# Optimization experiments

Measured on AMD Instinct MI355X. Metric: run time of the kernel, lower is better.

Reference implementation:

```python
import jax, jax.numpy as jnp
import numpy as np

KERNEL = 3
PAD = 1
STRIDE = 1

def setup_inputs() -> dict:
    key = jax.random.key(0)
    k1, k2 = jax.random.split(key)
    x = jax.random.normal(k1, (32, 128, 56, 56), dtype=jnp.float32)
    # xavier_uniform-like init for weight
    fan_in = 128 * KERNEL * KERNEL
    fan_out = 256 * KERNEL * KERNEL
    limit = float(np.sqrt(6.0 / (fan_in + fan_out)))
    weight = jax.random.uniform(k2, (256, 128, KERNEL, KERNEL), dtype=jnp.float32,
                                minval=-limit, maxval=limit)
    bias = jnp.zeros((256,), dtype=jnp.float32)
    return {"x": x, "weight": weight, "bias": bias}

def reference(x, weight, bias):
    # Equivalent to the per-pixel im2col matmul loop: a standard 3x3 conv,
    # stride 1, symmetric padding 1, plus per-channel bias.
    out = jax.lax.conv_general_dilated(
        x, weight,
        window_strides=(STRIDE, STRIDE),
        padding=((PAD, PAD), (PAD, PAD)),
        dimension_numbers=("NCHW", "OIHW", "NCHW"),
    )
    return out + bias[None, :, None, None]
```

## Files before the change

### kernel.cpp

```cpp
#include <hip/hip_runtime.h>
#include <hip/hip_bf16.h>
#include <stdint.h>
#include <stddef.h>

#define NIMG 32
#define C_IN 128
#define C_OUT 256
#define HW 56
#define SP 3136
#define STOT (NIMG * SP)
#define PD 58
#define KTOT 1152

#define BM 256
#define BN 256
#define BK 64
#define NKT (KTOT / BK)
#define THREADS 512

typedef __attribute__((ext_vector_type(8))) short bf16x8;
typedef __attribute__((ext_vector_type(4))) float f32x4;

__device__ __forceinline__ void gload16(const void* g, void* l) {
    __builtin_amdgcn_global_load_lds(
        (const __attribute__((address_space(1))) void*)g,
        (__attribute__((address_space(3))) void*)l,
        16, 0, 0);
}

#define BAR() do { asm volatile("" ::: "memory"); \
                   __builtin_amdgcn_s_barrier();  \
                   asm volatile("" ::: "memory"); } while (0)
#define LGKM0() do { asm volatile("s_waitcnt lgkmcnt(0)" ::: "memory"); \
                     __builtin_amdgcn_sched_barrier(0); } while (0)
#define VMCNT(n) do { asm volatile("s_waitcnt vmcnt(" #n ")" ::: "memory"); \
                      __builtin_amdgcn_sched_barrier(0); } while (0)

__device__ __forceinline__ unsigned short bf2u(float f) {
    __hip_bfloat16 b = __float2bfloat16(f);
    return *reinterpret_cast<unsigned short*>(&b);
}

__global__ __launch_bounds__(256)
void pad_transpose_kernel(const float* __restrict__ x,
                          __hip_bfloat16* __restrict__ xp) {
    __shared__ float t[C_IN][HW + 1];
    const int hp = blockIdx.x % PD;
    const int n  = blockIdx.x / PD;
    const int h  = hp - 1;
    const bool interior = ((unsigned)h < (unsigned)HW);
    if (interior) {
        for (int idx = threadIdx.x; idx < C_IN * HW; idx += 256) {
            int ci = idx / HW, w = idx - ci * HW;
            t[ci][w] = x[((size_t)n * C_IN + ci) * SP + h * HW + w];
        }
    }
    __syncthreads();
    ushort4* dst = (ushort4*)(xp + ((size_t)n * PD + hp) * PD * C_IN);
    for (int idx = threadIdx.x; idx < PD * C_IN / 4; idx += 256) {
        int el = idx * 4;
        int wp = el >> 7, c0 = el & 127;
        ushort4 v = {0, 0, 0, 0};
        if (interior && wp >= 1 && wp <= HW) {
            int w = wp - 1;
            v.x = bf2u(t[c0 + 0][w]);
            v.y = bf2u(t[c0 + 1][w]);
            v.z = bf2u(t[c0 + 2][w]);
            v.w = bf2u(t[c0 + 3][w]);
        }
        dst[idx] = v;
    }
}

__global__ void wt_transform_kernel(const float* __restrict__ wgt,
                                    __hip_bfloat16* __restrict__ wt) {
    int idx = blockIdx.x * 256 + threadIdx.x;
    int ci  = idx & 127;
    int co  = (idx >> 7) & 255;
    int tap = idx >> 15;
    wt[idx] = __float2bfloat16(wgt[(co * C_IN + ci) * 9 + tap]);
}

__global__ __launch_bounds__(THREADS, 2)
void conv_mfma_kernel(const __hip_bfloat16* __restrict__ xp,
                      const __hip_bfloat16* __restrict__ wt,
                      const float* __restrict__ bias,
                      float* __restrict__ out) {
    extern __shared__ short smem[];

    const int tid  = threadIdx.x;
    const int lane = tid & 63;
    const int wid  = tid >> 6;
    const int s0   = blockIdx.x * BN;

    const int cg_el = (((lane & 3) ^ ((lane >> 3) & 3)) << 3);
    const int srow  = wid * 16 + (lane >> 2);
    const int aS0   = srow * C_IN + cg_el;
    const int aS1   = aS0 + 128 * C_IN;
    int s_r = s0 + srow;
    int n_  = s_r / SP, rem = s_r - n_ * SP;
    int h_  = rem / HW, w_ = rem - h_ * HW;
    const int bS0 = ((n_ * PD + h_) * PD + w_) * C_IN + cg_el;
    s_r += 128;
    n_ = s_r / SP; rem = s_r - n_ * SP; h_ = rem / HW; w_ = rem - h_ * HW;
    const int bS1 = ((n_ * PD + h_) * PD + w_) * C_IN + cg_el;
    const int ldsw = wid * 512;

    const int rl  = lane & 15;
    const int rch = (((lane >> 4) ^ ((lane >> 1) & 3)) << 3);
    const int wm  = (wid >> 2) * 128;
    const int wn  = (wid & 3) * 64;
    const int aRd = (wm + rl) * 32 + rch;
    const int bRd = (wn + rl) * 32 + rch;

    auto STG_A = [&](int kt, int kk, int bf) {
        int t2 = (kt >= NKT) ? kt - NKT : kt;
        int tap = t2 >> 1;
        const __hip_bfloat16* src =
            wt + tap * (C_OUT * C_IN) + ((t2 & 1) << 6) + (kk << 5);
        short* d = smem + bf * 32768 + kk * 8192 + ldsw;
        gload16(src + aS0, d);
        gload16(src + aS1, d + 4096);
    };
    auto STG_B = [&](int kt, int kk, int bf) {
        int t2 = (kt >= NKT) ? kt - NKT : kt;
        int tap = t2 >> 1;
        int kh = (tap * 11) >> 5, kw = tap - kh * 3;
        const __hip_bfloat16* src =
            xp + (kh * PD + kw) * C_IN + ((t2 & 1) << 6) + (kk << 5);
        short* d = smem + bf * 32768 + 16384 + kk * 8192 + ldsw;
        gload16(src + bS0, d);
        gload16(src + bS1, d + 4096);
    };

    f32x4 acc[8][4] = {};

    STG_A(0, 0, 0); STG_B(0, 0, 0);
    STG_A(0, 1, 0); STG_B(0, 1, 0);
    STG_A(1, 0, 1); STG_B(1, 0, 1);
    VMCNT(4);
    BAR();

    for (int t = 0; t < NKT; ++t) {
        const int b = t & 1;
        const short* Ak0 = smem + b * 32768;
        const short* Ak1 = Ak0 + 8192;
        const short* Bk0 = Ak0 + 16384;
        const short* Bk1 = Ak0 + 24576;
        bf16x8 af[4], bfr[4];

        #pragma unroll
        for (int j = 0; j < 4; ++j) af[j]  = *(const bf16x8*)(Ak0 + aRd + j * 512);
        #pragma unroll
        for (int j = 0; j < 4; ++j) bfr[j] = *(const bf16x8*)(Bk0 + bRd + j * 512);
        STG_A(t + 1, 1, b ^ 1);
        BAR(); LGKM0();
        __builtin_amdgcn_s_setprio(1);
        #pragma unroll
        for (int mi = 0; mi < 4; ++mi)
            #pragma unroll
            for (int ni = 0; ni < 4; ++ni)
                acc[mi][ni] = __builtin_amdgcn_mfma_f32_16x16x32_bf16(
                    af[mi], bfr[ni], acc[mi][ni], 0, 0, 0);
        __builtin_amdgcn_s_setprio(0);
        BAR();

        #pragma unroll
        for (int j = 0; j < 4; ++j) af[j] = *(const bf16x8*)(Ak0 + aRd + 2048 + j * 512);
        STG_B(t + 1, 1, b ^ 1);
        BAR(); LGKM0();
        __builtin_amdgcn_s_setprio(1);
        #pragma unroll
        for (int mi = 0; mi < 4; ++mi)
            #pragma unroll
            for (int ni = 0; ni < 4; ++ni)
                acc[4 + mi][ni] = __builtin_amdgcn_mfma_f32_16x16x32_bf16(
                    af[mi], bfr[ni], acc[4 + mi][ni], 0, 0, 0);
        __builtin_amdgcn_s_setprio(0);
        BAR();

        #pragma unroll
        for (int j = 0; j < 4; ++j) af[j]  = *(const bf16x8*)(Ak1 + aRd + j * 512);
        #pragma unroll
        for (int j = 0; j < 4; ++j) bfr[j] = *(const bf16x8*)(Bk1 + bRd + j * 512);
        STG_A(t + 2, 0, b);
        BAR(); LGKM0();
        __builtin_amdgcn_s_setprio(1);
        #pragma unroll
        for (int mi = 0; mi < 4; ++mi)
            #pragma unroll
            for (int ni = 0; ni < 4; ++ni)
                acc[mi][ni] = __builtin_amdgcn_mfma_f32_16x16x32_bf16(
                    af[mi], bfr[ni], acc[mi][ni], 0, 0, 0);
        __builtin_amdgcn_s_setprio(0);
        BAR();

        #pragma unroll
        for (int j = 0; j < 4; ++j) af[j] = *(const bf16x8*)(Ak1 + aRd + 2048 + j * 512);
        STG_B(t + 2, 0, b);
        BAR(); LGKM0();
        __builtin_amdgcn_s_setprio(1);
        #pragma unroll
        for (int mi = 0; mi < 4; ++mi)
            #pragma unroll
            for (int ni = 0; ni < 4; ++ni)
                acc[4 + mi][ni] = __builtin_amdgcn_mfma_f32_16x16x32_bf16(
                    af[mi], bfr[ni], acc[4 + mi][ni], 0, 0, 0);
        __builtin_amdgcn_s_setprio(0);
        VMCNT(4);
        BAR();
    }

    #pragma unroll
    for (int ni = 0; ni < 4; ++ni) {
        int s  = s0 + wn + ni * 16 + rl;
        int n  = s / SP;
        int si = s - n * SP;
        float* obase = out + (size_t)n * C_OUT * SP + si;
        #pragma unroll
        for (int mi = 0; mi < 8; ++mi) {
            int cob = wm + mi * 16 + ((lane >> 4) << 2);
            #pragma unroll
            for (int j = 0; j < 4; ++j) {
                int co = cob + j;
                obase[(size_t)co * SP] = acc[mi][ni][j] + bias[co];
            }
        }
    }
}

__global__ void conv_direct_kernel(const float* __restrict__ x,
                                   const float* __restrict__ wgt,
                                   const float* __restrict__ bias,
                                   float* __restrict__ out) {
    long idx = (long)blockIdx.x * 256 + threadIdx.x;
    if (idx >= (long)NIMG * C_OUT * SP) return;
    int si = (int)(idx % SP);
    int co = (int)((idx / SP) % C_OUT);
    int n  = (int)(idx / ((long)SP * C_OUT));
    int h = si / HW, w = si - (si / HW) * HW;
    float acc = bias[co];
    for (int ci = 0; ci < C_IN; ++ci) {
        const float* xr = x + ((size_t)n * C_IN + ci) * SP;
        const float* wr = wgt + ((size_t)co * C_IN + ci) * 9;
        #pragma unroll
        for (int kh = 0; kh < 3; ++kh) {
            int ih = h + kh - 1;
            if (ih < 0 || ih >= HW) continue;
            #pragma unroll
            for (int kw = 0; kw < 3; ++kw) {
                int iw = w + kw - 1;
                if (iw < 0 || iw >= HW) continue;
                acc += xr[ih * HW + iw] * wr[kh * 3 + kw];
            }
        }
    }
    out[idx] = acc;
}

extern "C" void kernel_launch(void* const* d_in, const int* in_sizes, int n_in,
                              void* d_out, int out_size, void* d_ws, size_t ws_size,
                              hipStream_t stream) {
    const float* x    = (const float*)d_in[0];
    const float* wgt  = (const float*)d_in[1];
    const float* bias = (const float*)d_in[2];
    float* out = (float*)d_out;

    const size_t xp_bytes = (size_t)NIMG * PD * PD * C_IN * sizeof(__hip_bfloat16);
    const size_t wt_bytes = (size_t)9 * C_OUT * C_IN * sizeof(__hip_bfloat16);

    if (ws_size >= xp_bytes + wt_bytes) {
        __hip_bfloat16* xp  = (__hip_bfloat16*)d_ws;
        __hip_bfloat16* wtb = (__hip_bfloat16*)((char*)d_ws + xp_bytes);

        pad_transpose_kernel<<<NIMG * PD, 256, 0, stream>>>(x, xp);
        wt_transform_kernel<<<(9 * C_OUT * C_IN) / 256, 256, 0, stream>>>(wgt, wtb);

        hipFuncSetAttribute((const void*)conv_mfma_kernel,
                            hipFuncAttributeMaxDynamicSharedMemorySize, 131072);
        conv_mfma_kernel<<<STOT / BN, THREADS, 131072, stream>>>(xp, wtb, bias, out);
    } else {
        long total = (long)NIMG * C_OUT * SP;
        conv_direct_kernel<<<(int)((total + 255) / 256), 256, 0, stream>>>(
            x, wgt, bias, out);
    }
}
```

Baseline: 103.4 us.

## Retile conv GEMM to 256x224 with 4-stage LDS ring and register double-buffered fragments

Changes the output tile to 256 channels by 224 spatial positions, so the 100352 positions split evenly into 448 blocks with no tail and blocks are remapped in an XCD-aware order. The K loop moves from a two-buffer scheme with many barriers to a 4-slot LDS ring, with register-double-buffered fragments and partial lgkmcnt waits so LDS reads overlap MFMA. The warp layout becomes 4x2 with 4x7 MFMA tiles per wave, and bias is preloaded into registers. This raises register pressure, and the clamped second B row loads duplicate rows; both the host launch grid and the LDS size must match the new tiling.

```diff
diff --git a/kernel.cpp b/kernel.cpp
--- a/kernel.cpp
+++ b/kernel.cpp
@@ -13,7 +13,7 @@
 #define KTOT 1152
 
 #define BM 256
-#define BN 256
+#define BN 224
 #define BK 64
 #define NKT (KTOT / BK)
 #define THREADS 512
@@ -31,7 +31,7 @@
 #define BAR() do { asm volatile("" ::: "memory"); \
                    __builtin_amdgcn_s_barrier();  \
                    asm volatile("" ::: "memory"); } while (0)
-#define LGKM0() do { asm volatile("s_waitcnt lgkmcnt(0)" ::: "memory"); \
+#define LGKM(n) do { asm volatile("s_waitcnt lgkmcnt(" #n ")" ::: "memory"); \
                      __builtin_amdgcn_sched_barrier(0); } while (0)
 #define VMCNT(n) do { asm volatile("s_waitcnt vmcnt(" #n ")" ::: "memory"); \
                       __builtin_amdgcn_sched_barrier(0); } while (0)
@@ -91,7 +91,8 @@
     const int tid  = threadIdx.x;
     const int lane = tid & 63;
     const int wid  = tid >> 6;
-    const int s0   = blockIdx.x * BN;
+    const int wg   = (blockIdx.x & 7) * 56 + (blockIdx.x >> 3);
+    const int s0   = wg * BN;
 
     const int cg_el = (((lane & 3) ^ ((lane >> 3) & 3)) << 3);
     const int srow  = wid * 16 + (lane >> 2);
@@ -101,129 +102,102 @@
     int n_  = s_r / SP, rem = s_r - n_ * SP;
     int h_  = rem / HW, w_ = rem - h_ * HW;
     const int bS0 = ((n_ * PD + h_) * PD + w_) * C_IN + cg_el;
-    s_r += 128;
+    int srow2 = 128 + srow; if (srow2 > BN - 1) srow2 = BN - 1;
+    s_r = s0 + srow2;
     n_ = s_r / SP; rem = s_r - n_ * SP; h_ = rem / HW; w_ = rem - h_ * HW;
     const int bS1 = ((n_ * PD + h_) * PD + w_) * C_IN + cg_el;
     const int ldsw = wid * 512;
 
     const int rl  = lane & 15;
     const int rch = (((lane >> 4) ^ ((lane >> 1) & 3)) << 3);
-    const int wm  = (wid >> 2) * 128;
-    const int wn  = (wid & 3) * 64;
+    const int wm  = (wid >> 1) * 64;
+    const int wn  = (wid & 1) * 112;
     const int aRd = (wm + rl) * 32 + rch;
     const int bRd = (wn + rl) * 32 + rch;
 
-    auto STG_A = [&](int kt, int kk, int bf) {
-        int t2 = (kt >= NKT) ? kt - NKT : kt;
-        int tap = t2 >> 1;
-        const __hip_bfloat16* src =
-            wt + tap * (C_OUT * C_IN) + ((t2 & 1) << 6) + (kk << 5);
-        short* d = smem + bf * 32768 + kk * 8192 + ldsw;
-        gload16(src + aS0, d);
-        gload16(src + aS1, d + 4096);
+    auto STG = [&](int tau, int kk, int r) {
+        int tap = tau >> 1;
+        int ci0 = ((tau & 1) << 6) + (kk << 5);
+        const __hip_bfloat16* wsrc = wt + tap * (C_OUT * C_IN) + ci0;
+        short* Ad = smem + r * 16384 + ldsw;
+        gload16(wsrc + aS0, Ad);
+        gload16(wsrc + aS1, Ad + 4096);
+        int kh = (tap * 11) >> 5, kw = tap - kh * 3;
+        const __hip_bfloat16* xsrc = xp + (kh * PD + kw) * C_IN + ci0;
+        short* Bd = smem + r * 16384 + 8192 + ldsw;
+        gload16(xsrc + bS0, Bd);
+        gload16(xsrc + bS1, Bd + 4096);
     };
-    auto STG_B = [&](int kt, int kk, int bf) {
-        int t2 = (kt >= NKT) ? kt - NKT : kt;
-        int tap = t2 >> 1;
-        int kh = (tap * 11) >> 5, kw = tap - kh * 3;
-        const __hip_bfloat16* src =
-            xp + (kh * PD + kw) * C_IN + ((t2 & 1) << 6) + (kk << 5);
-        short* d = smem + bf * 32768 + 16384 + kk * 8192 + ldsw;
-        gload16(src + bS0, d);
-        gload16(src + bS1, d + 4096);
+    auto RD = [&](bf16x8* fa, bf16x8* fb, int r) {
+        const short* Ab = smem + r * 16384;
+        const short* Bb = Ab + 8192;
+        #pragma unroll
+        for (int j = 0; j < 4; ++j) fa[j] = *(const bf16x8*)(Ab + aRd + j * 512);
+        #pragma unroll
+        for (int j = 0; j < 7; ++j) fb[j] = *(const bf16x8*)(Bb + bRd + j * 512);
     };
 
-    f32x4 acc[8][4] = {};
-
-    STG_A(0, 0, 0); STG_B(0, 0, 0);
-    STG_A(0, 1, 0); STG_B(0, 1, 0);
-    STG_A(1, 0, 1); STG_B(1, 0, 1);
+    f32x4 acc[4][7] = {};
+    bf16x8 fa0[4], fb0[7], fa1[4], fb1[7];
+
+    #define MM(FA, FB) do { \
+        __builtin_amdgcn_s_setprio(1); \
+        _Pragma("unroll") \
+        for (int mi = 0; mi < 4; ++mi) \
+            _Pragma("unroll") \
+            for (int ni = 0; ni < 7; ++ni) \
+                acc[mi][ni] = __builtin_amdgcn_mfma_f32_16x16x32_bf16( \
+                    FA[mi], FB[ni], acc[mi][ni], 0, 0, 0); \
+        __builtin_amdgcn_s_setprio(0); \
+    } while (0)
+
+    STG(0, 0, 0); STG(0, 1, 1); STG(1, 0, 2);
     VMCNT(4);
     BAR();
+    RD(fa0, fb0, 0);
 
     for (int t = 0; t < NKT; ++t) {
-        const int b = t & 1;
-        const short* Ak0 = smem + b * 32768;
-        const short* Ak1 = Ak0 + 8192;
-        const short* Bk0 = Ak0 + 16384;
-        const short* Bk1 = Ak0 + 24576;
-        bf16x8 af[4], bfr[4];
-
-        #pragma unroll
-        for (int j = 0; j < 4; ++j) af[j]  = *(const bf16x8*)(Ak0 + aRd + j * 512);
-        #pragma unroll
-        for (int j = 0; j < 4; ++j) bfr[j] = *(const bf16x8*)(Bk0 + bRd + j * 512);
-        STG_A(t + 1, 1, b ^ 1);
-        BAR(); LGKM0();
-        __builtin_amdgcn_s_setprio(1);
-        #pragma unroll
-        for (int mi = 0; mi < 4; ++mi)
-            #pragma unroll
-            for (int ni = 0; ni < 4; ++ni)
-                acc[mi][ni] = __builtin_amdgcn_mfma_f32_16x16x32_bf16(
-                    af[mi], bfr[ni], acc[mi][ni], 0, 0, 0);
-        __builtin_amdgcn_s_setprio(0);
-        BAR();
-
-        #pragma unroll
-        for (int j = 0; j < 4; ++j) af[j] = *(const bf16x8*)(Ak0 + aRd + 2048 + j * 512);
-        STG_B(t + 1, 1, b ^ 1);
-        BAR(); LGKM0();
-        __builtin_amdgcn_s_setprio(1);
-        #pragma unroll
-        for (int mi = 0; mi < 4; ++mi)
-            #pragma unroll
-            for (int ni = 0; ni < 4; ++ni)
-                acc[4 + mi][ni] = __builtin_amdgcn_mfma_f32_16x16x32_bf16(
-                    af[mi], bfr[ni], acc[4 + mi][ni], 0, 0, 0);
-        __builtin_amdgcn_s_setprio(0);
-        BAR();
-
-        #pragma unroll
-        for (int j = 0; j < 4; ++j) af[j]  = *(const bf16x8*)(Ak1 + aRd + j * 512);
-        #pragma unroll
-        for (int j = 0; j < 4; ++j) bfr[j] = *(const bf16x8*)(Bk1 + bRd + j * 512);
-        STG_A(t + 2, 0, b);
-        BAR(); LGKM0();
-        __builtin_amdgcn_s_setprio(1);
-        #pragma unroll
-        for (int mi = 0; mi < 4; ++mi)
-            #pragma unroll
-            for (int ni = 0; ni < 4; ++ni)
-                acc[mi][ni] = __builtin_amdgcn_mfma_f32_16x16x32_bf16(
-                    af[mi], bfr[ni], acc[mi][ni], 0, 0, 0);
-        __builtin_amdgcn_s_setprio(0);
-        BAR();
-
-        #pragma unroll
-        for (int j = 0; j < 4; ++j) af[j] = *(const bf16x8*)(Ak1 + aRd + 2048 + j * 512);
-        STG_B(t + 2, 0, b);
-        BAR(); LGKM0();
-        __builtin_amdgcn_s_setprio(1);
-        #pragma unroll
-        for (int mi = 0; mi < 4; ++mi)
-            #pragma unroll
-            for (int ni = 0; ni < 4; ++ni)
-                acc[4 + mi][ni] = __builtin_amdgcn_mfma_f32_16x16x32_bf16(
-                    af[mi], bfr[ni], acc[4 + mi][ni], 0, 0, 0);
-        __builtin_amdgcn_s_setprio(0);
+        const int rb = (t & 1) << 1;
+
         VMCNT(4);
         BAR();
-    }
-
+        RD(fa1, fb1, rb + 1);
+        if (t <= 16) STG(t + 1, 1, (rb + 3) & 3);
+        LGKM(11);
+        MM(fa0, fb0);
+
+        VMCNT(4);
+        BAR();
+        if (t <= 16) {
+            RD(fa0, fb0, (rb + 2) & 3);
+            if (t <= 15) STG(t + 2, 0, rb);
+            LGKM(11);
+        } else {
+            LGKM(0);
+        }
+        MM(fa1, fb1);
+    }
+    #undef MM
+
+    float bv[4][4];
     #pragma unroll
-    for (int ni = 0; ni < 4; ++ni) {
+    for (int mi = 0; mi < 4; ++mi)
+        #pragma unroll
+        for (int j = 0; j < 4; ++j)
+            bv[mi][j] = bias[wm + mi * 16 + ((lane >> 4) << 2) + j];
+
+    #pragma unroll
+    for (int ni = 0; ni < 7; ++ni) {
         int s  = s0 + wn + ni * 16 + rl;
         int n  = s / SP;
         int si = s - n * SP;
         float* obase = out + (size_t)n * C_OUT * SP + si;
         #pragma unroll
-        for (int mi = 0; mi < 8; ++mi) {
+        for (int mi = 0; mi < 4; ++mi) {
             int cob = wm + mi * 16 + ((lane >> 4) << 2);
             #pragma unroll
             for (int j = 0; j < 4; ++j) {
-                int co = cob + j;
-                obase[(size_t)co * SP] = acc[mi][ni][j] + bias[co];
+                obase[(size_t)(cob + j) * SP] = acc[mi][ni][j] + bv[mi][j];
             }
         }
     }
```

Result: faster. 87.88 us (-15.0%).
